# Optimization experiments

Measured on AMD Instinct MI355X. Metric: run time of the kernel, lower is better.

The kernel has to match this reference:

```python
import jax, jax.numpy as jnp
from jax import lax
import numpy as np

K_TOP = 100
NMS_THRESH = 0.5
SUBJECT_CATEGORY_ID = 0


def box_cxcywh_to_xyxy(b):
    cx, cy, w, h = b[..., 0], b[..., 1], b[..., 2], b[..., 3]
    return jnp.stack([cx - 0.5 * w, cy - 0.5 * h, cx + 0.5 * w, cy + 0.5 * h], axis=-1)


def _pairwise_iou(boxes):
    # boxes: [K,4] xyxy; uses the +1 pixel convention from the original numpy NMS
    x1, y1, x2, y2 = boxes[:, 0], boxes[:, 1], boxes[:, 2], boxes[:, 3]
    area = (x2 - x1 + 1.0) * (y2 - y1 + 1.0)
    xx1 = jnp.maximum(x1[:, None], x1[None, :])
    yy1 = jnp.maximum(y1[:, None], y1[None, :])
    xx2 = jnp.minimum(x2[:, None], x2[None, :])
    yy2 = jnp.minimum(y2[:, None], y2[None, :])
    w = jnp.maximum(0.0, xx2 - xx1 + 1.0)
    h = jnp.maximum(0.0, yy2 - yy1 + 1.0)
    inter = w * h
    union = area[:, None] + area[None, :] - inter
    return inter / union


def _nms_keep(sub_boxes, obj_boxes, obj_labels, hoi_scores):
    # Greedy grouped pairwise NMS for one image.
    # Grouping key degenerates to object label (subject cat and verb-row are constant).
    K = sub_boxes.shape[0]
    max_scores = hoi_scores.max(axis=-1)
    order = jnp.argsort(-max_scores)
    ovr = _pairwise_iou(sub_boxes) * _pairwise_iou(obj_boxes)  # [K,K]
    same_group = obj_labels[:, None] == obj_labels[None, :]
    ovr = jnp.where(same_group, ovr, 0.0)
    ovr_s = ovr[order][:, order]
    upper = jnp.triu(jnp.ones((K, K), dtype=bool), k=1)
    sup_mat = (ovr_s > NMS_THRESH) & upper  # suppression only of later (lower-score) items

    def body(i, st):
        suppressed, keep = st
        ki = jnp.logical_not(suppressed[i])
        keep = keep.at[i].set(ki)
        suppressed = suppressed | (ki & sup_mat[i])
        return suppressed, keep

    _, keep_sorted = lax.fori_loop(0, K, body, (jnp.zeros(K, bool), jnp.zeros(K, bool)))
    return jnp.zeros(K, bool).at[order].set(keep_sorted)


def setup_inputs() -> dict:
    key = jax.random.key(0)
    k1, k2, k3, k4, k5, k6 = jax.random.split(key, 6)
    B, Q, C, V = 256, 300, 81, 117
    return {
        "pred_obj_logits": jax.random.normal(k1, (B, Q, C), dtype=jnp.float32),
        "pred_verb_logits": jax.random.normal(k2, (B, Q, V), dtype=jnp.float32),
        "pred_sub_boxes": jax.random.uniform(k3, (B, Q, 4), dtype=jnp.float32),
        "pred_obj_boxes": jax.random.uniform(k4, (B, Q, 4), dtype=jnp.float32),
        "correct_mat": (jax.random.uniform(k5, (V, C), dtype=jnp.float32) > 0.3).astype(jnp.float32),
        "target_sizes": jax.random.randint(k6, (B, 2), 200, 640, dtype=jnp.int32),
    }


def reference(pred_obj_logits, pred_verb_logits, pred_sub_boxes, pred_obj_boxes, correct_mat, target_sizes):
    B, Q, C = pred_obj_logits.shape
    V = pred_verb_logits.shape[-1]

    obj_prob = jax.nn.softmax(pred_obj_logits, axis=-1)       # [B,Q,C]  (no_obj=False)
    verb_scores = jax.nn.sigmoid(pred_verb_logits)            # [B,Q,V]

    topk_values, topk_indexes = lax.top_k(obj_prob.reshape(B, Q * C), K_TOP)  # [B,100]
    topk_boxes = topk_indexes // C
    obj_labels = topk_indexes % C

    vs = jnp.take_along_axis(verb_scores, topk_boxes[..., None], axis=1)      # [B,100,V]
    ob = jnp.take_along_axis(pred_obj_boxes, topk_boxes[..., None], axis=1)   # [B,100,4]
    sb = jnp.take_along_axis(pred_sub_boxes, topk_boxes[..., None], axis=1)

    img_h = target_sizes[:, 0].astype(jnp.float32)
    img_w = target_sizes[:, 1].astype(jnp.float32)
    scale_fct = jnp.stack([img_w, img_h, img_w, img_h], axis=1)  # [B,4]
    sub_boxes = box_cxcywh_to_xyxy(sb) * scale_fct[:, None, :]
    obj_boxes = box_cxcywh_to_xyxy(ob) * scale_fct[:, None, :]

    hoi_scores = vs * topk_values[..., None]                    # [B,100,V]
    # masks[b,k,v] = correct_mat[v, obj_labels[b,k]]
    masks = correct_mat.T[obj_labels]                           # [B,100,V]
    hoi_scores = hoi_scores * masks

    keep = jax.vmap(_nms_keep)(sub_boxes, obj_boxes, obj_labels, hoi_scores)  # [B,100] bool
    final_scores = hoi_scores * keep[..., None].astype(hoi_scores.dtype)

    return final_scores, topk_values, obj_labels, sub_boxes, obj_boxes, keep
```

## Files before the change

### kernel.cpp

```cpp
#include <hip/hip_runtime.h>
#include <cmath>

#pragma clang fp contract(off)

#define NT 1024
constexpr int B_ = 256, Q_ = 300, C_ = 81, V_ = 117, K_ = 100;
constexpr int QC_ = Q_ * C_;
constexpr int KV_ = K_ * V_;
constexpr int CAP = 1024;

using u32 = unsigned int;
using u64 = unsigned long long;
using u16 = unsigned short;
using u8  = unsigned char;

constexpr u32 PCUT_BITS = 0x3C000000u;
constexpr int BIN0 = 480;
constexpr int NB   = 64;

constexpr int OFF_HS   = 0;
constexpr int OFF_HIST = 46816;
constexpr int OFF_RMAX = OFF_HIST + 8192;
constexpr int OFF_RINV = OFF_RMAX + 1240;
constexpr int OFF_BSUB = OFF_RINV + 1240;
constexpr int OFF_BOBJ = OFF_BSUB + 1600;
constexpr int OFF_SUPR = OFF_BOBJ + 1600;
constexpr int OFF_SELV = OFF_SUPR + 1600;
constexpr int OFF_SELI = OFF_SELV + 400;
constexpr int OFF_MAXB = OFF_SELI + 400;
constexpr int OFF_ORD  = OFF_MAXB + 400;
constexpr int OFF_LAB  = OFF_ORD + 104;
constexpr int OFF_MISC = OFF_LAB + 104;
constexpr int SMEM_SZ  = OFF_MISC + 48;
static_assert(SMEM_SZ <= 65536, "LDS overflow");
static_assert((OFF_BSUB & 15) == 0 && (OFF_BOBJ & 15) == 0, "b128 align");
static_assert(OFF_HIST >= 46800, "cand/hs overlap");

__device__ __forceinline__ int RM(int r) { return r + (r >> 5); }

__device__ __forceinline__ u64 shfl_xor_u64(u64 v, int mask) {
    u32 lo = (u32)v, hi = (u32)(v >> 32);
    lo = (u32)__shfl_xor((int)lo, mask, 64);
    hi = (u32)__shfl_xor((int)hi, mask, 64);
    return ((u64)hi << 32) | lo;
}

template <int CTRL>
__device__ __forceinline__ int dpp_i(int x) {
    return __builtin_amdgcn_update_dpp(0, x, CTRL, 0xF, 0xF, true);
}
__device__ __forceinline__ float bfly16(float x){ return __int_as_float(__builtin_amdgcn_ds_swizzle(__float_as_int(x), 0x401F)); }
__device__ __forceinline__ float bfly8 (float x){ return __int_as_float(dpp_i<0x128>(__float_as_int(x))); }
__device__ __forceinline__ float bfly4 (float x){ return __int_as_float(__builtin_amdgcn_ds_swizzle(__float_as_int(x), 0x101F)); }
__device__ __forceinline__ float bfly2 (float x){ return __int_as_float(dpp_i<0x4E>(__float_as_int(x))); }
__device__ __forceinline__ float bfly1 (float x){ return __int_as_float(dpp_i<0xB1>(__float_as_int(x))); }
__device__ __forceinline__ int ibfly4(int x){ return __builtin_amdgcn_ds_swizzle(x, 0x101F); }
__device__ __forceinline__ int ibfly2(int x){ return dpp_i<0x4E>(x); }
__device__ __forceinline__ int ibfly1(int x){ return dpp_i<0xB1>(x); }

__device__ __forceinline__ float iou4(float4 a, float4 b, float areaSum) {
    float xx1 = fmaxf(a.x, b.x);
    float yy1 = fmaxf(a.y, b.y);
    float xx2 = fminf(a.z, b.z);
    float yy2 = fminf(a.w, b.w);
    float w = fmaxf(0.f, xx2 - xx1 + 1.f);
    float h = fmaxf(0.f, yy2 - yy1 + 1.f);
    float inter = w * h;
    return inter / (areaSum - inter);
}

__global__ __launch_bounds__(NT, 4) void hoi_kernel(
    const float* __restrict__ obj_logits,
    const float* __restrict__ verb_logits,
    const float* __restrict__ sub_boxes_in,
    const float* __restrict__ obj_boxes_in,
    const float* __restrict__ cm,
    const int*   __restrict__ tsizes,
    float* __restrict__ out)
{
    const int b = blockIdx.x;
    const int tid = threadIdx.x;

    __shared__ __align__(16) u8 smem[SMEM_SZ];
    float* hs      = (float*)(smem + OFF_HS);
    u32*   hist    = (u32*)(smem + OFF_HIST);
    u64*   cand    = (u64*)(smem + OFF_HIST);
    float* asub    = (float*)(smem + OFF_HIST);
    float* aobj    = (float*)(smem + OFF_HIST + 512);
    float* rowmax  = (float*)(smem + OFF_RMAX);
    float* rinv    = (float*)(smem + OFF_RINV);
    float (*bsub)[4]   = (float(*)[4])(smem + OFF_BSUB);
    float (*bobj)[4]   = (float(*)[4])(smem + OFF_BOBJ);
    u32   (*supcol)[4] = (u32(*)[4])(smem + OFF_SUPR);
    float* sel_val = (float*)(smem + OFF_SELV);
    u32*   sel_idx = (u32*)(smem + OFF_SELI);
    u32*   maxbits = (u32*)(smem + OFF_MAXB);
    u8*    order8  = (u8*)(smem + OFF_ORD);
    u8*    lab8    = (u8*)(smem + OFF_LAB);
    u32*   skeep     = (u32*)(smem + OFF_MISC);
    u32*   keep_bits = (u32*)(smem + OFF_MISC + 16);
    u32*   s_cnt     = (u32*)(smem + OFF_MISC + 32);
    int*   sT        = (int*)(smem + OFF_MISC + 36);
    u64*   wred    = (u64*)(smem + OFF_BOBJ);
    u64*   s_prev  = (u64*)(smem + OFF_SUPR);

    const float* lg = obj_logits + (size_t)b * QC_;

    if (tid < NB) hist[tid] = 0;
    if (tid == 0) *s_cnt = 0;
    __syncthreads();

    const int g = tid >> 5, l = tid & 31;
    const bool have2 = (l < C_ - 64);
    u32 cmask = 0;
    {
        float v0[10], v1[10], v2[10];
        #pragma unroll
        for (int s = 0; s < 10; ++s) {
            int r = g + 32 * s;
            const float* row = lg + (size_t)((r < Q_ ? r : Q_ - 1) * C_);
            v0[s] = row[l];
            v1[s] = row[l + 32];
            v2[s] = have2 ? row[l + 64] : -INFINITY;
        }
        float m[10];
        #pragma unroll
        for (int s = 0; s < 10; ++s) m[s] = fmaxf(fmaxf(v0[s], v1[s]), v2[s]);
        #pragma unroll
        for (int s = 0; s < 10; ++s) m[s] = fmaxf(m[s], bfly16(m[s]));
        #pragma unroll
        for (int s = 0; s < 10; ++s) m[s] = fmaxf(m[s], bfly8(m[s]));
        #pragma unroll
        for (int s = 0; s < 10; ++s) m[s] = fmaxf(m[s], bfly4(m[s]));
        #pragma unroll
        for (int s = 0; s < 10; ++s) m[s] = fmaxf(m[s], bfly2(m[s]));
        #pragma unroll
        for (int s = 0; s < 10; ++s) m[s] = fmaxf(m[s], bfly1(m[s]));
        float e0[10], e1[10], e2[10], sm[10];
        #pragma unroll
        for (int s = 0; s < 10; ++s) {
            e0[s] = expf(v0[s] - m[s]);
            e1[s] = expf(v1[s] - m[s]);
            e2[s] = have2 ? expf(v2[s] - m[s]) : 0.f;
            sm[s] = e0[s] + e1[s] + e2[s];
        }
        #pragma unroll
        for (int s = 0; s < 10; ++s) sm[s] += bfly16(sm[s]);
        #pragma unroll
        for (int s = 0; s < 10; ++s) sm[s] += bfly8(sm[s]);
        #pragma unroll
        for (int s = 0; s < 10; ++s) sm[s] += bfly4(sm[s]);
        #pragma unroll
        for (int s = 0; s < 10; ++s) sm[s] += bfly2(sm[s]);
        #pragma unroll
        for (int s = 0; s < 10; ++s) sm[s] += bfly1(sm[s]);
        #pragma unroll
        for (int s = 0; s < 10; ++s) {
            int r = g + 32 * s;
            if (r < Q_) {
                float ri = 1.f / sm[s];
                float p0 = e0[s] * ri, p1 = e1[s] * ri;
                u32 x0 = __float_as_uint(p0), x1 = __float_as_uint(p1);
                if (x0 >= PCUT_BITS) {
                    atomicAdd(&hist[(x0 >> 21) - BIN0], 1u);
                    cmask |= 1u << (3 * s);
                }
                if (x1 >= PCUT_BITS) {
                    atomicAdd(&hist[(x1 >> 21) - BIN0], 1u);
                    cmask |= 1u << (3 * s + 1);
                }
                if (have2) {
                    float p2 = e2[s] * ri;
                    u32 x2 = __float_as_uint(p2);
                    if (x2 >= PCUT_BITS) {
                        atomicAdd(&hist[(x2 >> 21) - BIN0], 1u);
                        cmask |= 1u << (3 * s + 2);
                    }
                }
                if (l == 0) { rowmax[RM(r)] = m[s]; rinv[RM(r)] = ri; }
            }
        }
    }
    __syncthreads();

    if (tid < 64) {
        u32 suf = hist[tid];
        #pragma unroll
        for (int off = 1; off < 64; off <<= 1) {
            u32 o = (u32)__shfl_down((int)suf, off, 64);
            suf += (tid + off < 64) ? o : 0;
        }
        u32 nxt = (u32)__shfl_down((int)suf, 1, 64);
        if (tid == 63) nxt = 0;
        if (suf >= (u32)K_ && nxt < (u32)K_) *sT = BIN0 + tid;
    }
    __syncthreads();
    const int T = *sT;

    u32 mk = cmask;
    while (mk) {
        int bpos = (int)__builtin_ctz(mk);
        mk &= mk - 1;
        int s = (bpos * 171) >> 9;
        int c = bpos - 3 * s;
        int r = g + 32 * s;
        int col = l + 32 * c;
        int i = r * C_ + col;
        float p = expf(lg[i] - rowmax[RM(r)]) * rinv[RM(r)];
        u32 xb = __float_as_uint(p);
        if ((int)(xb >> 21) >= T) {
            u32 pos = atomicAdd(s_cnt, 1u);
            if (pos < (u32)CAP)
                cand[pos] = ((u64)xb << 32) | (u32)(~i);
        }
    }
    __syncthreads();
    const int ncand = (int)*s_cnt;

    if (ncand <= CAP) {
        if (tid < ncand) {
            u64 mykey = cand[tid];
            int rank = 0;
            int f = 0;
            for (; f + 4 <= ncand; f += 4) {
                u64 k0 = cand[f], k1 = cand[f + 1];
                u64 k2 = cand[f + 2], k3 = cand[f + 3];
                rank += (k0 > mykey) ? 1 : 0;
                rank += (k1 > mykey) ? 1 : 0;
                rank += (k2 > mykey) ? 1 : 0;
                rank += (k3 > mykey) ? 1 : 0;
            }
            for (; f < ncand; ++f) rank += (cand[f] > mykey) ? 1 : 0;
            if (rank < K_) {
                sel_val[rank] = __uint_as_float((u32)(mykey >> 32));
                sel_idx[rank] = ~(u32)mykey;
            }
        }
    } else {
        if (tid == 0) *s_prev = ~0ull;
        __syncthreads();
        for (int r = 0; r < K_; r++) {
            u64 prev = *s_prev;
            u64 local = 0;
            for (int i = tid; i < QC_; i += NT) {
                int q = i / C_;
                float p = expf(lg[i] - rowmax[RM(q)]) * rinv[RM(q)];
                u64 key = ((u64)__float_as_uint(p) << 32) | (u32)(~i);
                if (key < prev && key > local) local = key;
            }
            for (int off = 32; off > 0; off >>= 1) {
                u64 o = shfl_xor_u64(local, off);
                if (o > local) local = o;
            }
            if ((tid & 63) == 0) wred[tid >> 6] = local;
            __syncthreads();
            if (tid == 0) {
                u64 m = wred[0];
                for (int wv = 1; wv < 16; wv++) if (wred[wv] > m) m = wred[wv];
                *s_prev = m;
                u32 idx = ~(u32)m;
                if (idx >= (u32)QC_) idx = 0;
                sel_val[r] = __uint_as_float((u32)(m >> 32));
                sel_idx[r] = idx;
            }
            __syncthreads();
        }
    }
    __syncthreads();

    if (tid < 800) {
        int c = tid >> 3, j = tid & 7;
        u32 idx = sel_idx[c];
        int q = (int)idx / C_, lab = (int)idx - q * C_;
        const float* vrow = verb_logits + ((size_t)b * Q_ + q) * V_;
        float sv = sel_val[c];
        float xv[15], cv[15];
        #pragma unroll
        for (int k = 0; k < 15; ++k) {
            int v = j + 8 * k;
            int vc = v < V_ ? v : V_ - 1;
            xv[k] = vrow[vc];
            cv[k] = cm[vc * C_ + lab];
        }
        float m = 0.f;
        #pragma unroll
        for (int k = 0; k < 15; ++k) {
            int v = j + 8 * k;
            if (v < V_) {
                float hv = (1.f / (1.f + expf(-xv[k]))) * sv * cv[k];
                hs[c * V_ + v] = hv;
                m = fmaxf(m, hv);
            }
        }
        m = fmaxf(m, bfly4(m));
        m = fmaxf(m, bfly2(m));
        m = fmaxf(m, bfly1(m));
        if (j == 0) { maxbits[c] = __float_as_uint(m); lab8[c] = (u8)lab; }
    } else if (tid < 900) {
        int t = tid - 800;
        int idx = (int)sel_idx[t];
        int q = idx / C_;
        float iw = (float)tsizes[b * 2 + 1];
        float ih = (float)tsizes[b * 2 + 0];
        float4 sb = ((const float4*)sub_boxes_in)[(size_t)b * Q_ + q];
        float x1 = (sb.x - 0.5f * sb.z) * iw, y1 = (sb.y - 0.5f * sb.w) * ih;
        float x2 = (sb.x + 0.5f * sb.z) * iw, y2 = (sb.y + 0.5f * sb.w) * ih;
        bsub[t][0] = x1; bsub[t][1] = y1; bsub[t][2] = x2; bsub[t][3] = y2;
        asub[t] = (x2 - x1 + 1.f) * (y2 - y1 + 1.f);
        supcol[t][0] = 0; supcol[t][1] = 0; supcol[t][2] = 0; supcol[t][3] = 0;
    } else if (tid < 1000) {
        int t = tid - 900;
        int idx = (int)sel_idx[t];
        int q = idx / C_;
        float iw = (float)tsizes[b * 2 + 1];
        float ih = (float)tsizes[b * 2 + 0];
        float4 ob = ((const float4*)obj_boxes_in)[(size_t)b * Q_ + q];
        float x1 = (ob.x - 0.5f * ob.z) * iw, y1 = (ob.y - 0.5f * ob.w) * ih;
        float x2 = (ob.x + 0.5f * ob.z) * iw, y2 = (ob.y + 0.5f * ob.w) * ih;
        bobj[t][0] = x1; bobj[t][1] = y1; bobj[t][2] = x2; bobj[t][3] = y2;
        aobj[t] = (x2 - x1 + 1.f) * (y2 - y1 + 1.f);
    } else if (tid < 1004) {
        keep_bits[tid - 1000] = 0;
    }
    __syncthreads();

    if (tid < 800) {
        int r = tid >> 3, j = tid & 7;
        u64 kr = ((u64)maxbits[r] << 32) | (u32)(~r);
        int rank = 0;
        for (int k = 0; k < 13; k++) {
            int jj = j * 13 + k;
            if (jj < K_) {
                u64 kj = ((u64)maxbits[jj] << 32) | (u32)(~jj);
                rank += (kj > kr) ? 1 : 0;
            }
        }
        rank += ibfly4(rank);
        rank += ibfly2(rank);
        rank += ibfly1(rank);
        if (j == 0) order8[rank] = (u8)r;
    }
    __syncthreads();

    float* o0 = out;
    float* o1 = out + (size_t)B_ * KV_;
    float* o2 = o1 + (size_t)B_ * K_;
    float* o3 = o2 + (size_t)B_ * K_;
    float* o4 = o3 + (size_t)B_ * K_ * 4;
    float* o5 = o4 + (size_t)B_ * K_ * 4;

    if (tid < K_) {
        o1[(size_t)b * K_ + tid] = sel_val[tid];
        o2[(size_t)b * K_ + tid] = (float)(sel_idx[tid] % (u32)C_);
    }
    if (tid >= 128 && tid < 128 + K_ * 4) {
        int t = tid - 128;
        int r = t >> 2, k = t & 3;
        o3[((size_t)b * K_) * 4 + t] = bsub[r][k];
        o4[((size_t)b * K_) * 4 + t] = bobj[r][k];
    }

    for (int e = tid; e < K_ * K_; e += NT) {
        int i = e / K_, j = e - i * K_;
        if (j > i) {
            int ri = order8[i], rj = order8[j];
            u32 li = lab8[ri], lj = lab8[rj];
            if (li == lj) {
                float4 s_i = *(const float4*)bsub[ri];
                float4 s_j = *(const float4*)bsub[rj];
                float4 b_i = *(const float4*)bobj[ri];
                float4 b_j = *(const float4*)bobj[rj];
                float o = iou4(s_i, s_j, asub[ri] + asub[rj]) *
                          iou4(b_i, b_j, aobj[ri] + aobj[rj]);
                if (o > 0.5f)
                    atomicOr(&supcol[j][i >> 5], 1u << (i & 31));
            }
        }
    }
    __syncthreads();

    if (tid < 64) {
        u32 cA[4], cB[4];
        #pragma unroll
        for (int w = 0; w < 4; ++w) cA[w] = supcol[tid][w];
        #pragma unroll
        for (int w = 0; w < 4; ++w) cB[w] = (tid < K_ - 64) ? supcol[tid + 64][w] : 0u;
        bool sA = false, sB = false;
        u32 km[4] = {0, 0, 0, 0};
        #pragma unroll
        for (int i = 0; i < 64; ++i) {
            u64 bal = __ballot(sA);
            if (!((bal >> i) & 1)) {
                km[i >> 5] |= 1u << (i & 31);
                sA = sA || ((cA[i >> 5] >> (i & 31)) & 1u);
                sB = sB || ((cB[i >> 5] >> (i & 31)) & 1u);
            }
        }
        #pragma unroll
        for (int i = 64; i < K_; ++i) {
            u64 bal = __ballot(sB);
            if (!((bal >> (i - 64)) & 1)) {
                km[i >> 5] |= 1u << (i & 31);
                sA = sA || ((cA[i >> 5] >> (i & 31)) & 1u);
                sB = sB || ((cB[i >> 5] >> (i & 31)) & 1u);
            }
        }
        if (tid == 0) { skeep[0] = km[0]; skeep[1] = km[1]; skeep[2] = km[2]; skeep[3] = km[3]; }
    }
    __syncthreads();
    if (tid < K_) {
        if ((skeep[tid >> 5] >> (tid & 31)) & 1u) {
            int r = order8[tid];
            atomicOr(&keep_bits[r >> 5], 1u << (r & 31));
        }
    }
    __syncthreads();

    constexpr int KV4_ = KV_ / 4;
    for (int f4 = tid; f4 < KV4_; f4 += NT) {
        int base = f4 * 4;
        float4 h = *(const float4*)(hs + base);
        int r0 = base / V_, m0 = base - r0 * V_;
        int r1 = r0 + ((m0 + 1) >= V_ ? 1 : 0);
        int r2 = r0 + ((m0 + 2) >= V_ ? 1 : 0);
        int r3 = r0 + ((m0 + 3) >= V_ ? 1 : 0);
        float4 o;
        o.x = ((keep_bits[r0 >> 5] >> (r0 & 31)) & 1u) ? h.x : 0.f;
        o.y = ((keep_bits[r1 >> 5] >> (r1 & 31)) & 1u) ? h.y : 0.f;
        o.z = ((keep_bits[r2 >> 5] >> (r2 & 31)) & 1u) ? h.z : 0.f;
        o.w = ((keep_bits[r3 >> 5] >> (r3 & 31)) & 1u) ? h.w : 0.f;
        *(float4*)(o0 + (size_t)b * KV_ + base) = o;
    }
    if (tid < K_) {
        bool kp = (keep_bits[tid >> 5] >> (tid & 31)) & 1u;
        o5[(size_t)b * K_ + tid] = kp ? 1.f : 0.f;
    }
}

extern "C" void kernel_launch(void* const* d_in, const int* in_sizes, int n_in,
                              void* d_out, int out_size, void* d_ws, size_t ws_size,
                              hipStream_t stream) {
    const float* obj_logits  = (const float*)d_in[0];
    const float* verb_logits = (const float*)d_in[1];
    const float* sub_boxes   = (const float*)d_in[2];
    const float* obj_boxes   = (const float*)d_in[3];
    const float* cm          = (const float*)d_in[4];
    const int*   ts          = (const int*)d_in[5];
    hipLaunchKernelGGL(hoi_kernel, dim3(B_), dim3(NT), 0, stream,
                       obj_logits, verb_logits, sub_boxes, obj_boxes, cm, ts,
                       (float*)d_out);
}
```

Measured before the change: 129.6 us.

## Stage correct_mat in LDS and write hoi scores straight to global

The whole correct_mat table is copied into LDS at kernel start, taking the space that used to hold the per-image hoi score buffer. Hoi scores are now written directly to the global output as they are computed. After NMS, only the rows that were suppressed are overwritten with zeros. This removes the LDS staging buffer and the scattered global reads of correct_mat. In exchange, each block loads about 38KB of cm, the verb-score writes become strided scalar stores instead of float4, and suppressed rows are written twice.

```diff
diff --git a/kernel.cpp b/kernel.cpp
--- a/kernel.cpp
+++ b/kernel.cpp
@@ -8,6 +8,7 @@
 constexpr int QC_ = Q_ * C_;
 constexpr int KV_ = K_ * V_;
 constexpr int CAP = 1024;
+constexpr int CMN = V_ * C_;
 
 using u32 = unsigned int;
 using u64 = unsigned long long;
@@ -18,8 +19,8 @@
 constexpr int BIN0 = 480;
 constexpr int NB   = 64;
 
-constexpr int OFF_HS   = 0;
-constexpr int OFF_HIST = 46816;
+constexpr int OFF_CM   = 0;
+constexpr int OFF_HIST = 37920;
 constexpr int OFF_RMAX = OFF_HIST + 8192;
 constexpr int OFF_RINV = OFF_RMAX + 1240;
 constexpr int OFF_BSUB = OFF_RINV + 1240;
@@ -34,7 +35,8 @@
 constexpr int SMEM_SZ  = OFF_MISC + 48;
 static_assert(SMEM_SZ <= 65536, "LDS overflow");
 static_assert((OFF_BSUB & 15) == 0 && (OFF_BOBJ & 15) == 0, "b128 align");
-static_assert(OFF_HIST >= 46800, "cand/hs overlap");
+static_assert(OFF_HIST >= OFF_CM + CMN * 4, "cm/hist overlap");
+static_assert((OFF_HIST & 7) == 0, "cand u64 align");
 
 __device__ __forceinline__ int RM(int r) { return r + (r >> 5); }
 
@@ -82,7 +84,7 @@
     const int tid = threadIdx.x;
 
     __shared__ __align__(16) u8 smem[SMEM_SZ];
-    float* hs      = (float*)(smem + OFF_HS);
+    float* cml     = (float*)(smem + OFF_CM);
     u32*   hist    = (u32*)(smem + OFF_HIST);
     u64*   cand    = (u64*)(smem + OFF_HIST);
     float* asub    = (float*)(smem + OFF_HIST);
@@ -106,8 +108,21 @@
 
     const float* lg = obj_logits + (size_t)b * QC_;
 
+    float* o0 = out;
+    float* o1 = out + (size_t)B_ * KV_;
+    float* o2 = o1 + (size_t)B_ * K_;
+    float* o3 = o2 + (size_t)B_ * K_;
+    float* o4 = o3 + (size_t)B_ * K_ * 4;
+    float* o5 = o4 + (size_t)B_ * K_ * 4;
+
     if (tid < NB) hist[tid] = 0;
     if (tid == 0) *s_cnt = 0;
+    {
+        constexpr int CM4 = CMN / 4;
+        for (int i = tid; i < CM4; i += NT)
+            ((float4*)cml)[i] = ((const float4*)cm)[i];
+        if (tid == 0) cml[CMN - 1] = cm[CMN - 1];
+    }
     __syncthreads();
 
     const int g = tid >> 5, l = tid & 31;
@@ -273,22 +288,17 @@
         u32 idx = sel_idx[c];
         int q = (int)idx / C_, lab = (int)idx - q * C_;
         const float* vrow = verb_logits + ((size_t)b * Q_ + q) * V_;
+        float* orow = o0 + (size_t)b * KV_ + c * V_;
         float sv = sel_val[c];
-        float xv[15], cv[15];
-        #pragma unroll
-        for (int k = 0; k < 15; ++k) {
-            int v = j + 8 * k;
-            int vc = v < V_ ? v : V_ - 1;
-            xv[k] = vrow[vc];
-            cv[k] = cm[vc * C_ + lab];
-        }
         float m = 0.f;
         #pragma unroll
         for (int k = 0; k < 15; ++k) {
             int v = j + 8 * k;
             if (v < V_) {
-                float hv = (1.f / (1.f + expf(-xv[k]))) * sv * cv[k];
-                hs[c * V_ + v] = hv;
+                float x = vrow[v];
+                float cv = cml[v * C_ + lab];
+                float hv = (1.f / (1.f + expf(-x))) * sv * cv;
+                orow[v] = hv;
                 m = fmaxf(m, hv);
             }
         }
@@ -342,13 +352,6 @@
     }
     __syncthreads();
 
-    float* o0 = out;
-    float* o1 = out + (size_t)B_ * KV_;
-    float* o2 = o1 + (size_t)B_ * K_;
-    float* o3 = o2 + (size_t)B_ * K_;
-    float* o4 = o3 + (size_t)B_ * K_ * 4;
-    float* o5 = o4 + (size_t)B_ * K_ * 4;
-
     if (tid < K_) {
         o1[(size_t)b * K_ + tid] = sel_val[tid];
         o2[(size_t)b * K_ + tid] = (float)(sel_idx[tid] % (u32)C_);
@@ -416,20 +419,10 @@
     }
     __syncthreads();
 
-    constexpr int KV4_ = KV_ / 4;
-    for (int f4 = tid; f4 < KV4_; f4 += NT) {
-        int base = f4 * 4;
-        float4 h = *(const float4*)(hs + base);
-        int r0 = base / V_, m0 = base - r0 * V_;
-        int r1 = r0 + ((m0 + 1) >= V_ ? 1 : 0);
-        int r2 = r0 + ((m0 + 2) >= V_ ? 1 : 0);
-        int r3 = r0 + ((m0 + 3) >= V_ ? 1 : 0);
-        float4 o;
-        o.x = ((keep_bits[r0 >> 5] >> (r0 & 31)) & 1u) ? h.x : 0.f;
-        o.y = ((keep_bits[r1 >> 5] >> (r1 & 31)) & 1u) ? h.y : 0.f;
-        o.z = ((keep_bits[r2 >> 5] >> (r2 & 31)) & 1u) ? h.z : 0.f;
-        o.w = ((keep_bits[r3 >> 5] >> (r3 & 31)) & 1u) ? h.w : 0.f;
-        *(float4*)(o0 + (size_t)b * KV_ + base) = o;
+    for (int f = tid; f < KV_; f += NT) {
+        int r = f / V_;
+        if (!((keep_bits[r >> 5] >> (r & 31)) & 1u))
+            o0[(size_t)b * KV_ + f] = 0.f;
     }
     if (tid < K_) {
         bool kp = (keep_bits[tid >> 5] >> (tid & 31)) & 1u;
```

New measurement: 127.6 us. About the same (-1.6%).
